# Kernel optimization log

Hardware: AMD Instinct MI355X
Metric: run time of the kernel (lower is better)

Reference implementation:

```python
import jax
import jax.numpy as jnp
from jax import lax
import numpy as np

E = 4          # num_experts
CIN = 128
COUT = 128
K = 3
STAT = 6
HID = 16       # router hidden width
STRIDE = 1
PAD = 1


def setup_inputs() -> dict:
    key = jax.random.key(0)
    ks = jax.random.split(key, 8)
    B, H, W = 32, 64, 64
    x = jax.random.normal(ks[0], (B, CIN, H, W), dtype=jnp.float32)
    scene_stats = jax.random.normal(ks[1], (B, STAT), dtype=jnp.float32)
    # router: Linear(stat_dim,16) -> ReLU -> Linear(16,E) -> Softmax
    W1 = jax.random.normal(ks[2], (HID, STAT), dtype=jnp.float32) * (1.0 / np.sqrt(STAT))
    b1 = jnp.zeros((HID,), dtype=jnp.float32)
    W2 = jax.random.normal(ks[3], (E, HID), dtype=jnp.float32) * (1.0 / np.sqrt(HID))
    b2 = jnp.zeros((E,), dtype=jnp.float32)
    weight_experts = jax.random.normal(ks[4], (E, COUT, CIN, K, K), dtype=jnp.float32) * 0.02
    bias_experts = jnp.zeros((E, COUT), dtype=jnp.float32)
    return {"x": x, "scene_stats": scene_stats, "W1": W1, "b1": b1,
            "W2": W2, "b2": b2, "weight_experts": weight_experts,
            "bias_experts": bias_experts}


def reference(x, scene_stats, W1, b1, W2, b2, weight_experts, bias_experts):
    B, Cin, H, W = x.shape
    Cout = weight_experts.shape[1]
    # router
    h = jax.nn.relu(scene_stats @ W1.T + b1)                 # [B, HID]
    routing = jax.nn.softmax(h @ W2.T + b2, axis=1)          # [B, E]
    # per-sample dynamic weights / bias
    dyn_w = jnp.einsum('bk,koihw->boihw', routing, weight_experts)  # [B,Cout,Cin,K,K]
    dyn_b = jnp.einsum('bk,ko->bo', routing, bias_experts)          # [B,Cout]
    # grouped conv with groups = B (each sample uses its own filter bank)
    x_r = x.reshape(1, B * Cin, H, W)
    w_r = dyn_w.reshape(B * Cout, Cin, K, K)
    out = lax.conv_general_dilated(
        x_r, w_r,
        window_strides=(STRIDE, STRIDE),
        padding=((PAD, PAD), (PAD, PAD)),
        feature_group_count=B,
        dimension_numbers=('NCHW', 'OIHW', 'NCHW'))
    out = out.reshape(B, Cout, out.shape[2], out.shape[3])
    return out + dyn_b[:, :, None, None]
```

## Files before the change

kernel.cpp:

```cpp
#include <hip/hip_runtime.h>
#include <hip/hip_bf16.h>


typedef short bf16x8 __attribute__((ext_vector_type(8)));
typedef float f32x4  __attribute__((ext_vector_type(4)));

#define VMWAIT(n) asm volatile("s_waitcnt vmcnt(" #n ")" ::: "memory")

static __device__ __forceinline__ unsigned short f2bf(float f) {
    unsigned u = __float_as_uint(f);
    u = u + 0x7FFFu + ((u >> 16) & 1u);
    return (unsigned short)(u >> 16);
}

static __device__ __forceinline__ void gl2lds16(const unsigned short* g, unsigned short* l) {
    __builtin_amdgcn_global_load_lds(
        (const __attribute__((address_space(1))) unsigned int*)g,
        (__attribute__((address_space(3))) unsigned int*)l,
        16, 0, 0);
}

__global__ void prep_kernel(const float* __restrict__ x, unsigned short* __restrict__ xbfT,
                            const float* __restrict__ stats, const float* __restrict__ W1,
                            const float* __restrict__ b1, const float* __restrict__ W2,
                            const float* __restrict__ b2, const float* __restrict__ wexp,
                            const float* __restrict__ bexp, unsigned short* __restrict__ dynw,
                            float* __restrict__ dynb)
{
    __shared__ float smem[4*1152 + 128];
    const int tid = threadIdx.x;

    if (blockIdx.x < 2112) {
        unsigned int* ls32 = (unsigned int*)smem;
        const int b  = blockIdx.x / 66;
        const int rr = blockIdx.x - b*66;
        const int gr = rr - 1;

        if (gr < 0 || gr > 63) {
            for (int cic = 0; cic < 4; ++cic) {
                int4* dst = (int4*)(xbfT + ((unsigned long long)((b*4 + cic)*66 + rr))*(66*32));
                for (int d = tid; d < 264; d += 256) dst[d] = make_int4(0,0,0,0);
            }
            return;
        }
        const int lane = tid & 63;
        const int w    = tid >> 6;
#pragma unroll
        for (int k = 0; k < 16; ++k) {
            int cp = w + 4*k;
            const float* p0 = x + (((unsigned long long)b*128 + 2*cp)*64 + gr)*64 + lane;
            unsigned lo = f2bf(p0[0]);
            unsigned hi = f2bf(p0[64*64]);
            ls32[cp*66 + lane] = lo | (hi << 16);
        }
        __syncthreads();
        for (int d = tid; d < 1056; d += 256) {
            int cic  = d / 264;
            int r    = d - cic*264;
            int lcol = r >> 2;
            int cg   = r & 3;
            int4 v;
            if (lcol == 0 || lcol == 65) {
                v = make_int4(0,0,0,0);
            } else {
                int col  = lcol - 1;
                int base = (cic*16 + cg*4)*66 + col;
                v.x = ls32[base];
                v.y = ls32[base + 66];
                v.z = ls32[base + 2*66];
                v.w = ls32[base + 3*66];
            }
            int p = (cg + (lcol >> 1)) & 3;
            int4* dst = (int4*)(xbfT + ((unsigned long long)((b*4 + cic)*66 + rr))*(66*32));
            dst[lcol*4 + p] = v;
        }
        return;
    }

    const int bid2 = blockIdx.x - 2112;
    const int co   = bid2 & 127;
    const int bg   = bid2 >> 7;
    float* ls = smem;
    float* lr = smem + 4*1152;

    if (tid < 32) {
        float s[6];
#pragma unroll
        for (int i = 0; i < 6; ++i) s[i] = stats[tid*6 + i];
        float h[16];
#pragma unroll
        for (int j = 0; j < 16; ++j) {
            float a = b1[j];
#pragma unroll
            for (int i = 0; i < 6; ++i) a += W1[j*6+i]*s[i];
            h[j] = a > 0.f ? a : 0.f;
        }
        float lg[4];
#pragma unroll
        for (int e = 0; e < 4; ++e) {
            float a = b2[e];
#pragma unroll
            for (int j = 0; j < 16; ++j) a += W2[e*16+j]*h[j];
            lg[e] = a;
        }
        float m = fmaxf(fmaxf(lg[0],lg[1]), fmaxf(lg[2],lg[3]));
        float ex[4], sum = 0.f;
#pragma unroll
        for (int e = 0; e < 4; ++e) { ex[e] = expf(lg[e]-m); sum += ex[e]; }
        float inv = 1.f / sum;
#pragma unroll
        for (int e = 0; e < 4; ++e) lr[tid*4+e] = ex[e]*inv;
    }
    for (int i = tid; i < 4*1152; i += 256) {
        int e = i / 1152, j = i - e*1152;
        ls[i] = wexp[((unsigned long long)(e*128 + co))*1152 + j];
    }
    __syncthreads();

    if (bg == 0 && tid < 32) {
        float sb = 0.f;
#pragma unroll
        for (int e = 0; e < 4; ++e) sb += lr[tid*4+e] * bexp[e*128 + co];
        dynb[tid*128 + co] = sb;
    }

    const int ci  = tid & 127;
    const int tp0 = tid >> 7;
    const int cic = ci >> 5;
    const int g   = (ci >> 3) & 3;
    const int jj  = ci & 7;
    const int mi  = co >> 4;
    const int l15 = co & 15;
    for (int bb = bg*8; bb < bg*8 + 8; ++bb) {
        float r0 = lr[bb*4+0], r1 = lr[bb*4+1], r2 = lr[bb*4+2], r3 = lr[bb*4+3];
#pragma unroll
        for (int pp = 0; pp < 5; ++pp) {
            int tap = 2*pp + tp0;
            if (tap < 9) {
                int j = ci*9 + tap;
                float v = r0*ls[j] + r1*ls[1152+j] + r2*ls[2*1152+j] + r3*ls[3*1152+j];
                dynw[((((unsigned long long)(bb*4 + cic)*9 + tap)*8 + mi)*64 + g*16 + l15)*8 + jj] = f2bf(v);
            }
        }
    }
}

__global__ __launch_bounds__(256, 2) void conv_kernel(
    const unsigned short* __restrict__ xbfT,
    const unsigned short* __restrict__ dynw,
    const float* __restrict__ dynb,
    float* __restrict__ out)
{
    __shared__ __align__(16) unsigned short xs[6*66*32];
    __shared__ __align__(16) unsigned short wsm[6][4096];

    const int tid  = threadIdx.x;
    const int wave = tid >> 6;
    const int lane = tid & 63;
    const int l15  = lane & 15;
    const int g    = lane >> 4;

    int bidx = ((blockIdx.x & 7) << 6) | (blockIdx.x >> 3);
    const int b  = bidx >> 4;
    const int r0 = (bidx & 15) << 2;

    f32x4 acc[8][4];
#pragma unroll
    for (int mi = 0; mi < 8; ++mi)
#pragma unroll
        for (int ni = 0; ni < 4; ++ni) acc[mi][ni] = (f32x4){0.f,0.f,0.f,0.f};

    const unsigned short* xsrcb = xbfT + (unsigned long long)b*(4ull*66*66*32);
    const unsigned short* wsrcb = dynw + (unsigned long long)b*(4ull*9*4096);

#pragma unroll
    for (int k = 0; k < 3; ++k) {
        const unsigned short* wsrc = wsrcb + (unsigned)(k*4096);
        gl2lds16(wsrc + (unsigned)tid*8,       wsm[k] + (unsigned)tid*8);
        gl2lds16(wsrc + (unsigned)(tid+256)*8, wsm[k] + (unsigned)(tid+256)*8);
    }
    {
        const unsigned short* src = xsrcb + (unsigned)r0*(66*32);
        for (int c = tid; c < 1584; c += 256) gl2lds16(src + c*8, xs + c*8);
    }
    __syncthreads();

#pragma unroll
    for (int p = 0; p < 12; ++p) {
        const int cic = p / 3;
        if (p > 0) {
            VMWAIT(0);
            __builtin_amdgcn_s_barrier();
            __builtin_amdgcn_sched_barrier(0);
        }
        const bool xreload = (p % 3) == 0 && p > 0;
        if (xreload) {
            const unsigned short* src = xsrcb + (unsigned)(cic*(66*66*32))
                                      + (unsigned)r0*(66*32);
            for (int c = tid; c < 1584; c += 256) gl2lds16(src + c*8, xs + c*8);
        }
        if (p < 11) {
#pragma unroll
            for (int k = 0; k < 3; ++k) {
                const int s = 3*p + 3 + k;
                const unsigned short* wsrc = wsrcb + (unsigned)(s*4096);
                unsigned short* wd = wsm[s % 6];
                gl2lds16(wsrc + (unsigned)tid*8,       wd + (unsigned)tid*8);
                gl2lds16(wsrc + (unsigned)(tid+256)*8, wd + (unsigned)(tid+256)*8);
            }
        }
        if (xreload) {
            if (p < 11) { VMWAIT(6); } else { VMWAIT(0); }
            __builtin_amdgcn_s_barrier();
            __builtin_amdgcn_sched_barrier(0);
        }
        const int ky   = p % 3;
        const int lrow = wave + ky;
        __builtin_amdgcn_s_setprio(1);
#pragma unroll
        for (int kx = 0; kx < 3; ++kx) {
            const unsigned short* wb = wsm[(3*p + kx) % 6];
            bf16x8 afrag[8];
#pragma unroll
            for (int mi = 0; mi < 8; ++mi)
                afrag[mi] = *(const bf16x8*)(wb + (unsigned)((mi*64 + lane)*8));
#pragma unroll
            for (int ni = 0; ni < 4; ++ni) {
                int lcol = 16*ni + l15 + kx;
                int boff = (lrow*66 + lcol)*64 + (((g + (lcol >> 1)) & 3) << 4);
                bf16x8 bfrag = *(const bf16x8*)((const char*)xs + boff);
#pragma unroll
                for (int mi = 0; mi < 8; ++mi)
                    acc[mi][ni] = __builtin_amdgcn_mfma_f32_16x16x32_bf16(
                                      afrag[mi], bfrag, acc[mi][ni], 0, 0, 0);
            }
        }
        __builtin_amdgcn_s_setprio(0);
    }

    const int y = r0 + wave;
#pragma unroll
    for (int mi = 0; mi < 8; ++mi) {
#pragma unroll
        for (int r = 0; r < 4; ++r) {
            int co = 16*mi + g*4 + r;
            float bias = dynb[b*128 + co];
            float* op = out + (((unsigned long long)(b*128 + co))*64 + y)*64;
#pragma unroll
            for (int ni = 0; ni < 4; ++ni)
                op[16*ni + l15] = acc[mi][ni][r] + bias;
        }
    }
}

extern "C" void kernel_launch(void* const* d_in, const int* in_sizes, int n_in,
                              void* d_out, int out_size, void* d_ws, size_t ws_size,
                              hipStream_t stream)
{
    const float* x     = (const float*)d_in[0];
    const float* stats = (const float*)d_in[1];
    const float* W1    = (const float*)d_in[2];
    const float* b1    = (const float*)d_in[3];
    const float* W2    = (const float*)d_in[4];
    const float* b2    = (const float*)d_in[5];
    const float* wexp  = (const float*)d_in[6];
    const float* bexp  = (const float*)d_in[7];
    float* out = (float*)d_out;

    char* ws = (char*)d_ws;
    float* dynb           = (float*)(ws + 512);
    unsigned short* dynw  = (unsigned short*)(ws + 32768);
    unsigned short* xbfT  = (unsigned short*)(ws + 32768 + 9437184);

    prep_kernel<<<2624, 256, 0, stream>>>(x, xbfT, stats, W1, b1, W2, b2,
                                          wexp, bexp, dynw, dynb);
    conv_kernel<<<512, 256, 0, stream>>>(xbfT, dynw, dynb, out);
}
```

Before: 65.66 us.

## Fuse fp32-to-bf16 input conversion and transposition into the conv kernel

Removes the separate prep pass that converted x to a padded, channel-interleaved bf16 buffer in workspace. The conv kernel now reads fp32 x directly with register loads, converts to bf16, shuffles across lanes into the swizzled LDS layout, and zeroes the halo columns itself, interleaving this with the weight prefetch. This drops a full write and re-read of the converted activation tensor. In exchange, each block reloads halo rows from fp32 (about 1.5x redundancy), the x stage becomes synchronous register loads instead of async global-to-LDS copies, and ALU and shuffle work is added to the conv kernel.

Result: faster. 59.58 us (-9.3%).

```diff
diff --git a/kernel.cpp b/kernel.cpp
--- a/kernel.cpp
+++ b/kernel.cpp
@@ -20,68 +20,17 @@
         16, 0, 0);
 }
 
-__global__ void prep_kernel(const float* __restrict__ x, unsigned short* __restrict__ xbfT,
-                            const float* __restrict__ stats, const float* __restrict__ W1,
+__global__ void prep_kernel(const float* __restrict__ stats, const float* __restrict__ W1,
                             const float* __restrict__ b1, const float* __restrict__ W2,
                             const float* __restrict__ b2, const float* __restrict__ wexp,
                             const float* __restrict__ bexp, unsigned short* __restrict__ dynw,
                             float* __restrict__ dynb)
 {
-    __shared__ float smem[4*1152 + 128];
+    __shared__ float ls[4*1152];
+    __shared__ float lr[32*4];
     const int tid = threadIdx.x;
-
-    if (blockIdx.x < 2112) {
-        unsigned int* ls32 = (unsigned int*)smem;
-        const int b  = blockIdx.x / 66;
-        const int rr = blockIdx.x - b*66;
-        const int gr = rr - 1;
-
-        if (gr < 0 || gr > 63) {
-            for (int cic = 0; cic < 4; ++cic) {
-                int4* dst = (int4*)(xbfT + ((unsigned long long)((b*4 + cic)*66 + rr))*(66*32));
-                for (int d = tid; d < 264; d += 256) dst[d] = make_int4(0,0,0,0);
-            }
-            return;
-        }
-        const int lane = tid & 63;
-        const int w    = tid >> 6;
-#pragma unroll
-        for (int k = 0; k < 16; ++k) {
-            int cp = w + 4*k;
-            const float* p0 = x + (((unsigned long long)b*128 + 2*cp)*64 + gr)*64 + lane;
-            unsigned lo = f2bf(p0[0]);
-            unsigned hi = f2bf(p0[64*64]);
-            ls32[cp*66 + lane] = lo | (hi << 16);
-        }
-        __syncthreads();
-        for (int d = tid; d < 1056; d += 256) {
-            int cic  = d / 264;
-            int r    = d - cic*264;
-            int lcol = r >> 2;
-            int cg   = r & 3;
-            int4 v;
-            if (lcol == 0 || lcol == 65) {
-                v = make_int4(0,0,0,0);
-            } else {
-                int col  = lcol - 1;
-                int base = (cic*16 + cg*4)*66 + col;
-                v.x = ls32[base];
-                v.y = ls32[base + 66];
-                v.z = ls32[base + 2*66];
-                v.w = ls32[base + 3*66];
-            }
-            int p = (cg + (lcol >> 1)) & 3;
-            int4* dst = (int4*)(xbfT + ((unsigned long long)((b*4 + cic)*66 + rr))*(66*32));
-            dst[lcol*4 + p] = v;
-        }
-        return;
-    }
-
-    const int bid2 = blockIdx.x - 2112;
-    const int co   = bid2 & 127;
-    const int bg   = bid2 >> 7;
-    float* ls = smem;
-    float* lr = smem + 4*1152;
+    const int co  = blockIdx.x & 127;
+    const int bg  = blockIdx.x >> 7;
 
     if (tid < 32) {
         float s[6];
@@ -146,7 +95,7 @@
 }
 
 __global__ __launch_bounds__(256, 2) void conv_kernel(
-    const unsigned short* __restrict__ xbfT,
+    const float* __restrict__ x,
     const unsigned short* __restrict__ dynw,
     const float* __restrict__ dynb,
     float* __restrict__ out)
@@ -159,6 +108,9 @@
     const int lane = tid & 63;
     const int l15  = lane & 15;
     const int g    = lane >> 4;
+    const int so    = tid & 7;
+    const int scg   = (tid >> 3) & 3;
+    const int scolO = (tid >> 5) & 7;
 
     int bidx = ((blockIdx.x & 7) << 6) | (blockIdx.x >> 3);
     const int b  = bidx >> 4;
@@ -170,19 +122,77 @@
 #pragma unroll
         for (int ni = 0; ni < 4; ++ni) acc[mi][ni] = (f32x4){0.f,0.f,0.f,0.f};
 
-    const unsigned short* xsrcb = xbfT + (unsigned long long)b*(4ull*66*66*32);
+    const float* xsrcb = x + (unsigned long long)b*(128ull*64*64);
     const unsigned short* wsrcb = dynw + (unsigned long long)b*(4ull*9*4096);
 
-#pragma unroll
-    for (int k = 0; k < 3; ++k) {
-        const unsigned short* wsrc = wsrcb + (unsigned)(k*4096);
-        gl2lds16(wsrc + (unsigned)tid*8,       wsm[k] + (unsigned)tid*8);
-        gl2lds16(wsrc + (unsigned)(tid+256)*8, wsm[k] + (unsigned)(tid+256)*8);
-    }
-    {
-        const unsigned short* src = xsrcb + (unsigned)r0*(66*32);
-        for (int c = tid; c < 1584; c += 256) gl2lds16(src + c*8, xs + c*8);
-    }
+#define XISSUE(kk)                                                             \
+    do {                                                                       \
+        int grow_ = r0 + (kk) - 1;                                             \
+        int growc_ = grow_ < 0 ? 0 : (grow_ > 63 ? 63 : grow_);                \
+        const float* xp_ = xsrcb + (((unsigned long long)(cic_*32 + scg*8 + so))*64 \
+                            + growc_)*64 + scolO*8;                            \
+        xv[(kk)%3][0] = *(const float4*)xp_;                                   \
+        xv[(kk)%3][1] = *(const float4*)(xp_ + 4);                             \
+    } while (0)
+
+#define XPROC(kk)                                                              \
+    do {                                                                       \
+        int grow_ = r0 + (kk) - 1;                                             \
+        bool oob_ = (grow_ < 0) || (grow_ > 63);                               \
+        float4 v0 = xv[(kk)%3][0], v1 = xv[(kk)%3][1];                         \
+        unsigned ra = oob_ ? 0u : (f2bf(v0.x) | ((unsigned)f2bf(v0.y) << 16)); \
+        unsigned rb = oob_ ? 0u : (f2bf(v0.z) | ((unsigned)f2bf(v0.w) << 16)); \
+        unsigned rc = oob_ ? 0u : (f2bf(v1.x) | ((unsigned)f2bf(v1.y) << 16)); \
+        unsigned rd = oob_ ? 0u : (f2bf(v1.z) | ((unsigned)f2bf(v1.w) << 16)); \
+        unsigned pa = __shfl_xor(ra,1), pb = __shfl_xor(rb,1);                 \
+        unsigned pc = __shfl_xor(rc,1), pd = __shfl_xor(rd,1);                 \
+        bool oddl = so & 1;                                                    \
+        unsigned sa = oddl ? ((pa>>16)|(ra&0xFFFF0000u)) : ((ra&0xFFFFu)|(pa<<16)); \
+        unsigned sb = oddl ? ((pb>>16)|(rb&0xFFFF0000u)) : ((rb&0xFFFFu)|(pb<<16)); \
+        unsigned sc = oddl ? ((pc>>16)|(rc&0xFFFF0000u)) : ((rc&0xFFFFu)|(pc<<16)); \
+        unsigned sd = oddl ? ((pd>>16)|(rd&0xFFFF0000u)) : ((rd&0xFFFFu)|(pd<<16)); \
+        unsigned qa = __shfl_xor(sa,2), qb = __shfl_xor(sb,2);                 \
+        unsigned qc = __shfl_xor(sc,2), qd = __shfl_xor(sd,2);                 \
+        bool hi2 = so & 2;                                                     \
+        unsigned A0 = hi2 ? qc : sa, A1 = hi2 ? sc : qa;                       \
+        unsigned B0 = hi2 ? qd : sb, B1 = hi2 ? sd : qb;                       \
+        int cA_ = (so & 1) + (hi2 ? 4 : 0);                                    \
+        int half8_ = (so >> 2) << 3;                                           \
+        int lcolA_ = scolO*8 + cA_ + 1;                                        \
+        int lcolB_ = lcolA_ + 2;                                               \
+        int byteA_ = ((kk)*66 + lcolA_)*64 + (((scg + (lcolA_>>1)) & 3)<<4) + half8_; \
+        int byteB_ = ((kk)*66 + lcolB_)*64 + (((scg + (lcolB_>>1)) & 3)<<4) + half8_; \
+        *(uint2*)((char*)xs + byteA_) = make_uint2(A0, A1);                    \
+        *(uint2*)((char*)xs + byteB_) = make_uint2(B0, B1);                    \
+    } while (0)
+
+#define XSTAGE(CIC_, WFIRST_, DRAIN_)                                          \
+    do {                                                                       \
+        const int cic_ = (CIC_);                                               \
+        float4 xv[3][2];                                                       \
+        XISSUE(0); XISSUE(1);                                                  \
+        _Pragma("unroll")                                                      \
+        for (int t = 0; t < 3; ++t) {                                          \
+            const unsigned short* wsrc_ = wsrcb + (unsigned)(((WFIRST_) + t)*4096); \
+            unsigned short* wd_ = wsm[((WFIRST_) + t) % 6];                    \
+            gl2lds16(wsrc_ + (unsigned)tid*8,       wd_ + (unsigned)tid*8);    \
+            gl2lds16(wsrc_ + (unsigned)(tid+256)*8, wd_ + (unsigned)(tid+256)*8); \
+        }                                                                      \
+        VMWAIT(8); XPROC(0); XISSUE(2);                                        \
+        VMWAIT(8); XPROC(1); XISSUE(3);                                        \
+        VMWAIT(8); XPROC(2); XISSUE(4);                                        \
+        VMWAIT(8); XPROC(3); XISSUE(5);                                        \
+        VMWAIT(8); XPROC(4);                                                   \
+        if (DRAIN_) { VMWAIT(0); } else { VMWAIT(6); }                         \
+        XPROC(5);                                                              \
+    } while (0)
+
+    if (tid < 48) {
+        int zrow = tid >> 3, zcol = ((tid >> 2) & 1) ? 65 : 0, zch = tid & 3;
+        *(uint4*)((char*)xs + (zrow*66 + zcol)*64 + zch*16) = make_uint4(0,0,0,0);
+    }
+    XSTAGE(0, 0, true);
+    asm volatile("s_waitcnt lgkmcnt(0)" ::: "memory");
     __syncthreads();
 
 #pragma unroll
@@ -193,27 +203,21 @@
             __builtin_amdgcn_s_barrier();
             __builtin_amdgcn_sched_barrier(0);
         }
-        const bool xreload = (p % 3) == 0 && p > 0;
-        if (xreload) {
-            const unsigned short* src = xsrcb + (unsigned)(cic*(66*66*32))
-                                      + (unsigned)r0*(66*32);
-            for (int c = tid; c < 1584; c += 256) gl2lds16(src + c*8, xs + c*8);
-        }
-        if (p < 11) {
-#pragma unroll
-            for (int k = 0; k < 3; ++k) {
-                const int s = 3*p + 3 + k;
+        if ((p % 3) == 0 && p > 0) {
+            XSTAGE(cic, 3*p + 3, false);
+            asm volatile("s_waitcnt lgkmcnt(0)" ::: "memory");
+            __builtin_amdgcn_s_barrier();
+            __builtin_amdgcn_sched_barrier(0);
+        } else if (p < 11) {
+#pragma unroll
+            for (int t = 0; t < 3; ++t) {
+                const int s = 3*p + 3 + t;
                 const unsigned short* wsrc = wsrcb + (unsigned)(s*4096);
                 unsigned short* wd = wsm[s % 6];
                 gl2lds16(wsrc + (unsigned)tid*8,       wd + (unsigned)tid*8);
                 gl2lds16(wsrc + (unsigned)(tid+256)*8, wd + (unsigned)(tid+256)*8);
             }
         }
-        if (xreload) {
-            if (p < 11) { VMWAIT(6); } else { VMWAIT(0); }
-            __builtin_amdgcn_s_barrier();
-            __builtin_amdgcn_sched_barrier(0);
-        }
         const int ky   = p % 3;
         const int lrow = wave + ky;
         __builtin_amdgcn_s_setprio(1);
@@ -251,6 +255,9 @@
                 op[16*ni + l15] = acc[mi][ni][r] + bias;
         }
     }
+#undef XSTAGE
+#undef XPROC
+#undef XISSUE
 }
 
 extern "C" void kernel_launch(void* const* d_in, const int* in_sizes, int n_in,
@@ -270,9 +277,7 @@
     char* ws = (char*)d_ws;
     float* dynb           = (float*)(ws + 512);
     unsigned short* dynw  = (unsigned short*)(ws + 32768);
-    unsigned short* xbfT  = (unsigned short*)(ws + 32768 + 9437184);
-
-    prep_kernel<<<2624, 256, 0, stream>>>(x, xbfT, stats, W1, b1, W2, b2,
-                                          wexp, bexp, dynw, dynb);
-    conv_kernel<<<512, 256, 0, stream>>>(xbfT, dynw, dynb, out);
-}
+
+    prep_kernel<<<512, 256, 0, stream>>>(stats, W1, b1, W2, b2, wexp, bexp, dynw, dynb);
+    conv_kernel<<<512, 256, 0, stream>>>(x, dynw, dynb, out);
+}
```
